# Kernel optimization log

Measured on AMD Instinct MI355X. Metric: run time of the kernel, lower is better.

The kernel has to match this reference:

```python
import jax, jax.numpy as jnp
import numpy as np

HEADS = 8
GROUPS = 32
EPS = 1e-5


def setup_inputs() -> dict:
    key = jax.random.key(0)
    k_x, k_qkv, k_proj = jax.random.split(key, 3)
    B, C, H, W = 16, 512, 32, 32
    s = 0.02  # init scale for weights
    return {
        "x": jax.random.normal(k_x, (B, C, H, W), jnp.float32),
        "gn_scale": jnp.ones((C,), jnp.float32),
        "gn_bias": jnp.zeros((C,), jnp.float32),
        "w_qkv": jax.random.normal(k_qkv, (3 * C, C), jnp.float32) * s,
        "b_qkv": jnp.zeros((3 * C,), jnp.float32),
        "w_proj": jax.random.normal(k_proj, (C, C), jnp.float32) * s,
        "b_proj": jnp.zeros((C,), jnp.float32),
    }


def _group_norm(x, scale, bias):
    # x: [B, C, T]; GroupNorm32 computes stats in fp32
    B, C, T = x.shape
    xg = x.reshape(B, GROUPS, C // GROUPS, T).astype(jnp.float32)
    mu = xg.mean(axis=(2, 3), keepdims=True)
    var = xg.var(axis=(2, 3), keepdims=True)
    xn = ((xg - mu) * jax.lax.rsqrt(var + EPS)).reshape(B, C, T)
    return xn * scale[None, :, None] + bias[None, :, None]


def reference(x, gn_scale, gn_bias, w_qkv, b_qkv, w_proj, b_proj):
    B, C = x.shape[0], x.shape[1]
    T = int(np.prod(x.shape[2:]))
    xf = x.reshape(B, C, T)
    xn = _group_norm(xf, gn_scale, gn_bias).astype(x.dtype)
    # 1x1 conv == per-position matmul: [B, 3C, T]
    qkv = jnp.einsum('oc,bct->bot', w_qkv, xn) + b_qkv[None, :, None]
    ch = C // HEADS
    qkv = qkv.reshape(B * HEADS, 3 * ch, T)
    q, k, v = jnp.split(qkv, 3, axis=1)  # each [B*H, ch, T]
    scale = ch ** -0.25
    # scores: [B*H, T, T], softmax in fp32 (matches weight.float())
    w = jnp.einsum('bct,bcs->bts', q * scale, k * scale)
    w = jax.nn.softmax(w.astype(jnp.float32), axis=-1).astype(q.dtype)
    a = jnp.einsum('bts,bcs->bct', w, v).reshape(B, C, T)
    h = jnp.einsum('oc,bct->bot', w_proj, a) + b_proj[None, :, None]
    return (xf + h).reshape(x.shape)
```

## Files before the change

### kernel.cpp

```cpp
#include <hip/hip_runtime.h>
#include <cstdint>

#define NB 16
#define NC 512
#define NT 1024
#define NH 8
#define NG 32
#define GN_EPS 1e-5f
#define KSOFT 0.18033688011112042f

typedef float  f32x16 __attribute__((ext_vector_type(16)));
typedef __bf16 bf16x8 __attribute__((ext_vector_type(8)));
typedef unsigned int uint32x4 __attribute__((ext_vector_type(4)));

static __device__ __forceinline__ f32x16 zero16() {
    f32x16 z;
    #pragma unroll
    for (int i = 0; i < 16; ++i) z[i] = 0.f;
    return z;
}

static __device__ __forceinline__ f32x16 mfma(bf16x8 a, bf16x8 b, f32x16 c) {
    return __builtin_amdgcn_mfma_f32_32x32x16_bf16(a, b, c, 0, 0, 0);
}

static __device__ __forceinline__ unsigned pk2(float a, float b) {
    unsigned short x = __builtin_bit_cast(unsigned short, (__bf16)a);
    unsigned short y = __builtin_bit_cast(unsigned short, (__bf16)b);
    return (unsigned)x | ((unsigned)y << 16);
}

static __device__ __forceinline__ void swap32(unsigned& a, unsigned& b) {
#if __has_builtin(__builtin_amdgcn_permlane32_swap)
    auto r = __builtin_amdgcn_permlane32_swap(a, b, false, false);
    a = r[0];
    b = r[1];
#else
    unsigned sa = __shfl_xor(a, 32), sb = __shfl_xor(b, 32);
    bool hi = (threadIdx.x & 32) != 0;
    unsigned na = hi ? sb : a;
    unsigned nb = hi ? b : sa;
    a = na; b = nb;
#endif
}

static __device__ __forceinline__ bf16x8 lds_frag(const __bf16* base, int row, int sb) {
    const char* p = (const char*)base + row * 128 + (sb ^ ((row & 7) << 4));
    return *(const bf16x8*)p;
}

#define GLOAD16(gp, lp)                                                        \
    __builtin_amdgcn_global_load_lds(                                          \
        (const __attribute__((address_space(1))) unsigned int*)(gp),           \
        (__attribute__((address_space(3))) unsigned int*)(lp), 16, 0, 0)

__global__ __launch_bounds__(256) void fused_pre(
        const float* __restrict__ x, const float* __restrict__ gs,
        const float* __restrict__ gb, const float* __restrict__ w_qkv,
        const float* __restrict__ w_proj, __bf16* __restrict__ xnT,
        __bf16* __restrict__ wq_bf, __bf16* __restrict__ wp_bf)
{
    const int blk = blockIdx.x;
    const int thr = threadIdx.x;
    if (blk >= 128) {
        int i = (blk - 128) * 256 + thr;
        const float* src;
        __bf16* dst;
        if (i < 196608) { src = w_qkv; dst = wq_bf; }
        else            { i -= 196608; src = w_proj; dst = wp_bf; }
        float4 f = ((const float4*)src)[i];
        uint2 u;
        u.x = pk2(f.x, f.y);
        u.y = pk2(f.z, f.w);
        ((uint2*)dst)[i] = u;
        return;
    }
    const int b = blk >> 3, c0 = (blk & 7) * 64;
    __shared__ float gstat[8];
    {
        const int wv = thr >> 6, lane = thr & 63;
        const float* base = x + ((size_t)b * NC + c0 + wv * 16) * NT;
        float s = 0.f, s2 = 0.f;
        #pragma unroll
        for (int ch = 0; ch < 16; ++ch) {
            const float4* r4 = (const float4*)(base + (size_t)ch * NT);
            #pragma unroll
            for (int p = 0; p < 4; ++p) {
                float4 v = r4[lane + p * 64];
                s += v.x + v.y + v.z + v.w;
                s2 = fmaf(v.x, v.x, fmaf(v.y, v.y, fmaf(v.z, v.z, fmaf(v.w, v.w, s2))));
            }
        }
        #pragma unroll
        for (int off = 32; off; off >>= 1) {
            s  += __shfl_down(s, off);
            s2 += __shfl_down(s2, off);
        }
        if (lane == 0) {
            const float inv_n = 1.f / 16384.f;
            float mu  = s * inv_n;
            float var = s2 * inv_n - mu * mu;
            gstat[wv]     = mu;
            gstat[wv + 4] = rsqrtf(var + GN_EPS);
        }
    }
    __syncthreads();
    __shared__ float xs[64][65];
    const int tloc = thr & 63;
    for (int t0 = 0; t0 < NT; t0 += 64) {
        #pragma unroll
        for (int p = 0; p < 16; ++p) {
            int cr = p * 4 + (thr >> 6);
            int c = c0 + cr;
            float mu = gstat[cr >> 4];
            float rs = gstat[(cr >> 4) + 4];
            float v = x[((size_t)b * NC + c) * NT + t0 + tloc];
            xs[cr][tloc] = (v - mu) * rs * gs[c] + gb[c];
        }
        __syncthreads();
        const int cd = thr & 31;
        #pragma unroll
        for (int pp = 0; pp < 8; ++pp) {
            int tr = pp * 8 + (thr >> 5);
            unsigned w = pk2(xs[2 * cd][tr], xs[2 * cd + 1][tr]);
            size_t off = ((size_t)b * NT + t0 + tr) * NC + c0 + 2 * cd;
            *(unsigned*)((char*)xnT + off * 2) = w;
        }
        __syncthreads();
    }
}

__global__ __launch_bounds__(256) void qkv_gemm(const __bf16* __restrict__ wq,
                                                const __bf16* __restrict__ xnT,
                                                const float* __restrict__ bias,
                                                __bf16* __restrict__ qv,
                                                __bf16* __restrict__ kT)
{
    const int b = blockIdx.z, o0 = blockIdx.y * 128, t0 = blockIdx.x * 128;
    __shared__ __align__(16) char smem[32768];
    __bf16* wt = (__bf16*)smem;
    __bf16* xt = (__bf16*)(smem + 16384);
    const int thr = threadIdx.x;
    const int lane = thr & 63, wv = thr >> 6;
    const int lr = lane & 31, h = lane >> 5;
    const int wo = (wv >> 1) * 64, wn = (wv & 1) * 64;
    f32x16 acc[2][2];
    #pragma unroll
    for (int i = 0; i < 2; ++i)
        #pragma unroll
        for (int j = 0; j < 2; ++j) acc[i][j] = zero16();

    for (int kb = 0; kb < 8; ++kb) {
        const int c0 = kb * 64;
        __syncthreads();
        #pragma unroll
        for (int p = 0; p < 4; ++p) {
            int idx = p * 256 + thr, row = idx >> 3, sl = idx & 7;
            GLOAD16(wq + (size_t)(o0 + row) * NC + c0 + 8 * (sl ^ (row & 7)), wt + idx * 8);
            GLOAD16(xnT + ((size_t)b * NT + t0 + row) * NC + c0 + 8 * (sl ^ (row & 7)), xt + idx * 8);
        }
        asm volatile("s_waitcnt vmcnt(0)" ::: "memory");
        __syncthreads();
        #pragma unroll
        for (int kc = 0; kc < 4; ++kc) {
            bf16x8 a0 = lds_frag(wt, wo + lr,      32 * kc + 16 * h);
            bf16x8 a1 = lds_frag(wt, wo + 32 + lr, 32 * kc + 16 * h);
            bf16x8 b0 = lds_frag(xt, wn + lr,      32 * kc + 16 * h);
            bf16x8 b1 = lds_frag(xt, wn + 32 + lr, 32 * kc + 16 * h);
            acc[0][0] = mfma(a0, b0, acc[0][0]);
            acc[0][1] = mfma(a0, b1, acc[0][1]);
            acc[1][0] = mfma(a1, b0, acc[1][0]);
            acc[1][1] = mfma(a1, b1, acc[1][1]);
        }
    }

    char* ktile = smem;
    #pragma unroll
    for (int mt = 0; mt < 2; ++mt) {
        const int X = o0 + wo + 32 * mt;
        const int xm = X % 192;
        const int cat = xm >> 6;
        const int hd = X / 192;
        if (cat != 1) {
            #pragma unroll
            for (int nt = 0; nt < 2; ++nt)
                #pragma unroll
                for (int r = 0; r < 16; ++r) {
                    int off = (r & 3) + 8 * (r >> 2) + 4 * h;
                    int o = X + off;
                    int row = (cat == 0) ? (xm + off) : (xm - 64 + off);
                    int t = t0 + wn + 32 * nt + lr;
                    float v = acc[mt][nt][r] + bias[o];
                    if (cat == 0) v *= KSOFT;
                    qv[((size_t)(b * 8 + hd) * 128 + row) * NT + t] = (__bf16)v;
                }
        }
    }
    __syncthreads();
    #pragma unroll
    for (int mt = 0; mt < 2; ++mt) {
        const int X = o0 + wo + 32 * mt;
        const int xm = X % 192;
        if ((xm >> 6) == 1) {
            #pragma unroll
            for (int nt = 0; nt < 2; ++nt) {
                int t_local = wn + 32 * nt + lr;
                #pragma unroll
                for (int g = 0; g < 4; ++g) {
                    int ob = X + 8 * g + 4 * h;
                    int cb = (xm - 64) + 8 * g + 4 * h;
                    uint2 d;
                    d.x = pk2(acc[mt][nt][4 * g + 0] + bias[ob + 0],
                              acc[mt][nt][4 * g + 1] + bias[ob + 1]);
                    d.y = pk2(acc[mt][nt][4 * g + 2] + bias[ob + 2],
                              acc[mt][nt][4 * g + 3] + bias[ob + 3]);
                    *(uint2*)(ktile + t_local * 144 + cb * 2) = d;
                }
            }
        }
    }
    if ((o0 % 192) != 128) {
        __syncthreads();
        const int khd = o0 / 192;
        #pragma unroll
        for (int pass = 0; pass < 4; ++pass) {
            int t_local = pass * 32 + (thr >> 3);
            int c8 = thr & 7;
            uint32x4 d = *(const uint32x4*)(ktile + t_local * 144 + c8 * 16);
            *(uint32x4*)(kT + ((size_t)(b * 8 + khd) * 1024 + t0 + t_local) * 64 + c8 * 8) = d;
        }
    }
}

#define PP(R) ((R) < 16 ? p0[(R) & 15] : p1[(R) & 15])

__global__ __launch_bounds__(512, 4) void attn_mfma(const __bf16* __restrict__ qv,
                                                    const __bf16* __restrict__ kT,
                                                    __bf16* __restrict__ aT)
{
    const int wg = blockIdx.x;
    const int orig = (wg & 7) * 64 + (wg >> 3);
    const int tq0 = (orig & 3) * 256;
    const int bh = orig >> 2;
    const int b = bh >> 3, hd = bh & 7;
    const __bf16* qg = qv + (size_t)bh * 128 * NT;
    const __bf16* vg = qg + (size_t)64 * NT;
    const __bf16* kTg = kT + (size_t)bh * 1024 * 64;
    const int thr = threadIdx.x, lane = thr & 63, wv = thr >> 6;
    const int lr = lane & 31, h = lane >> 5;
    const int tw = tq0 + wv * 32;
    __shared__ __align__(16) char smem[49152];

    bf16x8 qf[4];
    {
        const unsigned short* qs = (const unsigned short*)qg;
        #pragma unroll
        for (int kc = 0; kc < 4; ++kc) {
            unsigned w[4];
            #pragma unroll
            for (int ww = 0; ww < 4; ++ww) {
                int c0 = 16 * kc + 8 * h + 2 * ww;
                unsigned lo = qs[(size_t)c0 * NT + tw + lr];
                unsigned hi = qs[(size_t)(c0 + 1) * NT + tw + lr];
                w[ww] = lo | (hi << 16);
            }
            uint32x4 u = {w[0], w[1], w[2], w[3]};
            qf[kc] = __builtin_bit_cast(bf16x8, u);
        }
    }
    bf16x8 ones;
    #pragma unroll
    for (int i = 0; i < 8; ++i) ones[i] = (__bf16)1.0f;

    f32x16 oacc0 = zero16(), oacc1 = zero16(), sacc = zero16();

    const int row = thr >> 3, sl = thr & 7;
    const __bf16* kbase = kTg + (size_t)row * 64 + 8 * (sl ^ (row & 7));
    const __bf16* vbase = vg + (size_t)row * NT + 8 * (sl ^ (row & 7));
    const int ldsoff = thr * 8;

    GLOAD16(kbase,           (__bf16*)(smem)         + ldsoff);
    GLOAD16(vbase,           (__bf16*)(smem + 24576) + ldsoff);
    GLOAD16(kbase + 64 * 64, (__bf16*)(smem + 8192)  + ldsoff);
    GLOAD16(vbase + 64,      (__bf16*)(smem + 32768) + ldsoff);

    int cur = 0;
    for (int it = 0; it < 16; ++it) {
        __bf16* kcur = (__bf16*)(smem + cur * 8192);
        __bf16* vcur = (__bf16*)(smem + 24576 + cur * 8192);
        if (it < 14) {
            int nxt = cur + 2;
            if (nxt >= 3) nxt -= 3;
            const int s0 = (it + 2) * 64;
            GLOAD16(kbase + (size_t)s0 * 64, (__bf16*)(smem + nxt * 8192) + ldsoff);
            GLOAD16(vbase + s0,              (__bf16*)(smem + 24576 + nxt * 8192) + ldsoff);
            asm volatile("s_waitcnt vmcnt(8)" ::: "memory");
        } else if (it == 14) {
            asm volatile("s_waitcnt vmcnt(4)" ::: "memory");
        } else {
            asm volatile("s_waitcnt vmcnt(0)" ::: "memory");
        }
        __builtin_amdgcn_s_barrier();

        f32x16 p0 = zero16(), p1 = zero16();
        __builtin_amdgcn_s_setprio(1);
        #pragma unroll
        for (int kc = 0; kc < 4; ++kc) {
            bf16x8 ka0 = lds_frag(kcur, lr,      32 * kc + 16 * h);
            bf16x8 ka1 = lds_frag(kcur, 32 + lr, 32 * kc + 16 * h);
            p0 = mfma(ka0, qf[kc], p0);
            p1 = mfma(ka1, qf[kc], p1);
        }
        __builtin_amdgcn_s_setprio(0);

        #pragma unroll
        for (int r = 0; r < 16; ++r) {
            p0[r] = exp2f(p0[r]);
            p1[r] = exp2f(p1[r]);
        }

        #pragma unroll
        for (int ks = 0; ks < 4; ++ks) {
            const int Rb = 16 * (ks >> 1) + 8 * (ks & 1);
            unsigned a0 = pk2(PP(Rb + 0), PP(Rb + 1));
            unsigned c0 = pk2(PP(Rb + 2), PP(Rb + 3));
            unsigned a1 = pk2(PP(Rb + 4), PP(Rb + 5));
            unsigned c1 = pk2(PP(Rb + 6), PP(Rb + 7));
            swap32(a0, a1);
            swap32(c0, c1);
            uint32x4 u = {a0, c0, a1, c1};
            bf16x8 pf = __builtin_bit_cast(bf16x8, u);
            bf16x8 v0 = lds_frag(vcur, lr,      32 * ks + 16 * h);
            bf16x8 v1 = lds_frag(vcur, 32 + lr, 32 * ks + 16 * h);
            __builtin_amdgcn_s_setprio(1);
            oacc0 = mfma(v0, pf, oacc0);
            oacc1 = mfma(v1, pf, oacc1);
            sacc  = mfma(ones, pf, sacc);
            __builtin_amdgcn_s_setprio(0);
        }
        __builtin_amdgcn_s_barrier();
        ++cur;
        if (cur == 3) cur = 0;
    }

    float inv = 1.f / sacc[0];
    char* at = smem;
    {
        int t_local = wv * 32 + lr;
        #pragma unroll
        for (int g = 0; g < 4; ++g) {
            int cb = 8 * g + 4 * h;
            uint2 d0, d1;
            d0.x = pk2(oacc0[4 * g + 0] * inv, oacc0[4 * g + 1] * inv);
            d0.y = pk2(oacc0[4 * g + 2] * inv, oacc0[4 * g + 3] * inv);
            *(uint2*)(at + t_local * 144 + cb * 2) = d0;
            d1.x = pk2(oacc1[4 * g + 0] * inv, oacc1[4 * g + 1] * inv);
            d1.y = pk2(oacc1[4 * g + 2] * inv, oacc1[4 * g + 3] * inv);
            *(uint2*)(at + t_local * 144 + (cb + 32) * 2) = d1;
        }
    }
    __syncthreads();
    #pragma unroll
    for (int pass = 0; pass < 4; ++pass) {
        int t_local = pass * 64 + (thr >> 3);
        int c8 = thr & 7;
        uint32x4 d = *(const uint32x4*)(at + t_local * 144 + c8 * 16);
        *(uint32x4*)(aT + ((size_t)b * NT + tq0 + t_local) * NC + hd * 64 + c8 * 8) = d;
    }
}

__global__ __launch_bounds__(256) void proj_gemm(const __bf16* __restrict__ wp,
                                                 const __bf16* __restrict__ aT,
                                                 const float* __restrict__ bias,
                                                 const float* __restrict__ x,
                                                 float* __restrict__ out)
{
    const int b = blockIdx.z, o0 = blockIdx.y * 128, t0 = blockIdx.x * 128;
    __shared__ __align__(16) char smem[32768];
    __bf16* wt = (__bf16*)smem;
    __bf16* xt = (__bf16*)(smem + 16384);
    const int thr = threadIdx.x;
    const int lane = thr & 63, wv = thr >> 6;
    const int lr = lane & 31, h = lane >> 5;
    const int wo = (wv >> 1) * 64, wn = (wv & 1) * 64;
    f32x16 acc[2][2];
    #pragma unroll
    for (int i = 0; i < 2; ++i)
        #pragma unroll
        for (int j = 0; j < 2; ++j) acc[i][j] = zero16();

    for (int kb = 0; kb < 8; ++kb) {
        const int c0 = kb * 64;
        __syncthreads();
        #pragma unroll
        for (int p = 0; p < 4; ++p) {
            int idx = p * 256 + thr, row = idx >> 3, sl = idx & 7;
            GLOAD16(wp + (size_t)(o0 + row) * NC + c0 + 8 * (sl ^ (row & 7)), wt + idx * 8);
            GLOAD16(aT + ((size_t)b * NT + t0 + row) * NC + c0 + 8 * (sl ^ (row & 7)), xt + idx * 8);
        }
        asm volatile("s_waitcnt vmcnt(0)" ::: "memory");
        __syncthreads();
        #pragma unroll
        for (int kc = 0; kc < 4; ++kc) {
            bf16x8 a0 = lds_frag(wt, wo + lr,      32 * kc + 16 * h);
            bf16x8 a1 = lds_frag(wt, wo + 32 + lr, 32 * kc + 16 * h);
            bf16x8 b0 = lds_frag(xt, wn + lr,      32 * kc + 16 * h);
            bf16x8 b1 = lds_frag(xt, wn + 32 + lr, 32 * kc + 16 * h);
            acc[0][0] = mfma(a0, b0, acc[0][0]);
            acc[0][1] = mfma(a0, b1, acc[0][1]);
            acc[1][0] = mfma(a1, b0, acc[1][0]);
            acc[1][1] = mfma(a1, b1, acc[1][1]);
        }
    }
    #pragma unroll
    for (int mt = 0; mt < 2; ++mt)
        #pragma unroll
        for (int nt = 0; nt < 2; ++nt)
            #pragma unroll
            for (int r = 0; r < 16; ++r) {
                int o = o0 + wo + 32 * mt + (r & 3) + 8 * (r >> 2) + 4 * h;
                int t = t0 + wn + 32 * nt + lr;
                size_t off = ((size_t)b * NC + o) * NT + t;
                out[off] = acc[mt][nt][r] + bias[o] + x[off];
            }
}

extern "C" void kernel_launch(void* const* d_in, const int* in_sizes, int n_in,
                              void* d_out, int out_size, void* d_ws, size_t ws_size,
                              hipStream_t stream)
{
    const float* x       = (const float*)d_in[0];
    const float* gnscale = (const float*)d_in[1];
    const float* gnbias  = (const float*)d_in[2];
    const float* w_qkv   = (const float*)d_in[3];
    const float* b_qkv   = (const float*)d_in[4];
    const float* w_proj  = (const float*)d_in[5];
    const float* b_proj  = (const float*)d_in[6];
    float* out = (float*)d_out;

    char* ws = (char*)d_ws;
    __bf16* wq_bf = (__bf16*)(ws + 4096);
    __bf16* wp_bf = (__bf16*)(ws + 1576960);
    __bf16* xnT   = (__bf16*)(ws + 2101248);
    __bf16* qv    = (__bf16*)(ws + 18878464);
    __bf16* kTb   = (__bf16*)(ws + 52432896);
    __bf16* aTb   = (__bf16*)(ws + 69210112);

    fused_pre<<<1152, 256, 0, stream>>>(x, gnscale, gnbias, w_qkv, w_proj,
                                        xnT, wq_bf, wp_bf);
    qkv_gemm<<<dim3(8, 12, NB), 256, 0, stream>>>(wq_bf, xnT, b_qkv, qv, kTb);
    attn_mfma<<<512, 512, 0, stream>>>(qv, kTb, aTb);
    proj_gemm<<<dim3(8, 4, NB), 256, 0, stream>>>(wp_bf, aTb, b_proj, x, out);
}
```

Measured before the change: 144.4 us.

## Software-pipeline QK^T across key tiles to overlap exp2 with MFMA

```diff
diff --git a/kernel.cpp b/kernel.cpp
--- a/kernel.cpp
+++ b/kernel.cpp
@@ -232,7 +232,7 @@
     }
 }
 
-#define PP(R) ((R) < 16 ? p0[(R) & 15] : p1[(R) & 15])
+#define PP(R) ((R) < 16 ? pl[(R) & 15] : ph[(R) & 15])
 
 __global__ __launch_bounds__(512, 4) void attn_mfma(const __bf16* __restrict__ qv,
                                                     const __bf16* __restrict__ kT,
@@ -284,40 +284,59 @@
     GLOAD16(kbase + 64 * 64, (__bf16*)(smem + 8192)  + ldsoff);
     GLOAD16(vbase + 64,      (__bf16*)(smem + 32768) + ldsoff);
 
-    int cur = 0;
-    for (int it = 0; it < 16; ++it) {
-        __bf16* kcur = (__bf16*)(smem + cur * 8192);
-        __bf16* vcur = (__bf16*)(smem + 24576 + cur * 8192);
-        if (it < 14) {
-            int nxt = cur + 2;
-            if (nxt >= 3) nxt -= 3;
-            const int s0 = (it + 2) * 64;
-            GLOAD16(kbase + (size_t)s0 * 64, (__bf16*)(smem + nxt * 8192) + ldsoff);
-            GLOAD16(vbase + s0,              (__bf16*)(smem + 24576 + nxt * 8192) + ldsoff);
-            asm volatile("s_waitcnt vmcnt(8)" ::: "memory");
-        } else if (it == 14) {
-            asm volatile("s_waitcnt vmcnt(4)" ::: "memory");
+    asm volatile("s_waitcnt vmcnt(3)" ::: "memory");
+    __builtin_amdgcn_s_barrier();
+
+    f32x16 pl = zero16();
+    {
+        __bf16* k0 = (__bf16*)smem;
+        __builtin_amdgcn_s_setprio(1);
+        #pragma unroll
+        for (int kc = 0; kc < 4; ++kc)
+            pl = mfma(lds_frag(k0, lr, 32 * kc + 16 * h), qf[kc], pl);
+        __builtin_amdgcn_s_setprio(0);
+    }
+
+    int sV = 0;
+    for (int j = 0; j < 16; ++j) {
+        int sK = sV + 1; if (sK == 3) sK = 0;
+        int sW = sK + 1; if (sW == 3) sW = 0;
+        if (j < 15) {
+            asm volatile("s_waitcnt vmcnt(1)" ::: "memory");
         } else {
             asm volatile("s_waitcnt vmcnt(0)" ::: "memory");
         }
         __builtin_amdgcn_s_barrier();
-
-        f32x16 p0 = zero16(), p1 = zero16();
+        if (j < 14) {
+            const int s0 = (j + 2) * 64;
+            GLOAD16(kbase + (size_t)s0 * 64, (__bf16*)(smem + sW * 8192) + ldsoff);
+            GLOAD16(vbase + s0,              (__bf16*)(smem + 24576 + sW * 8192) + ldsoff);
+        }
+        __bf16* kcur = (__bf16*)(smem + sV * 8192);
+        __bf16* vcur = (__bf16*)(smem + 24576 + sV * 8192);
+
+        f32x16 ph = zero16();
         __builtin_amdgcn_s_setprio(1);
         #pragma unroll
-        for (int kc = 0; kc < 4; ++kc) {
-            bf16x8 ka0 = lds_frag(kcur, lr,      32 * kc + 16 * h);
-            bf16x8 ka1 = lds_frag(kcur, 32 + lr, 32 * kc + 16 * h);
-            p0 = mfma(ka0, qf[kc], p0);
-            p1 = mfma(ka1, qf[kc], p1);
-        }
+        for (int kc = 0; kc < 4; ++kc)
+            ph = mfma(lds_frag(kcur, 32 + lr, 32 * kc + 16 * h), qf[kc], ph);
         __builtin_amdgcn_s_setprio(0);
 
         #pragma unroll
-        for (int r = 0; r < 16; ++r) {
-            p0[r] = exp2f(p0[r]);
-            p1[r] = exp2f(p1[r]);
-        }
+        for (int r = 0; r < 16; ++r) pl[r] = exp2f(pl[r]);
+
+        f32x16 pln = zero16();
+        if (j < 15) {
+            __bf16* knxt = (__bf16*)(smem + sK * 8192);
+            __builtin_amdgcn_s_setprio(1);
+            #pragma unroll
+            for (int kc = 0; kc < 4; ++kc)
+                pln = mfma(lds_frag(knxt, lr, 32 * kc + 16 * h), qf[kc], pln);
+            __builtin_amdgcn_s_setprio(0);
+        }
+
+        #pragma unroll
+        for (int r = 0; r < 16; ++r) ph[r] = exp2f(ph[r]);
 
         #pragma unroll
         for (int ks = 0; ks < 4; ++ks) {
@@ -339,8 +358,8 @@
             __builtin_amdgcn_s_setprio(0);
         }
         __builtin_amdgcn_s_barrier();
-        ++cur;
-        if (cur == 3) cur = 0;
+        pl = pln;
+        sV = sK;
     }
 
     float inv = 1.f / sacc[0];
```

After: 168.9 us. +17.0%, slower.
